# Performance work log

Measured on AMD Instinct MI355X. Metric: run time of the kernel, lower is better.

## Reference

```python
import jax, jax.numpy as jnp
import numpy as np
from jax import lax

N, CIN, H, W = 32, 128, 64, 64
COUT, KH, KW = 256, 3, 3
STRIDE = (1, 1)
PADDING = ((1, 1), (1, 1))


def setup_inputs() -> dict:
    key = jax.random.key(0)
    k1, k2, k3, k4 = jax.random.split(key, 4)
    # binary input in {0,1}
    x = jax.random.randint(k1, (N, CIN, H, W), 0, 2).astype(jnp.float32)
    # ternary weight in {-1,0,1}
    weight = (jax.random.randint(k2, (COUT, CIN, KH, KW), 0, 3) - 1).astype(jnp.float32)
    # integer bias (folded from BN, floored to int per get_sign_bias_from_bn)
    bias = jax.random.randint(k3, (COUT,), -200, 200).astype(jnp.float32)
    # sign in {-1,+1}, broadcast shape (1, COUT, 1, 1)
    sign = jnp.where(jax.random.bernoulli(k4, 0.5, (1, COUT, 1, 1)), 1.0, -1.0).astype(jnp.float32)
    return {"x": x, "weight": weight, "bias": bias, "sign": sign}


def reference(x, weight, bias, sign):
    # y = conv2d(x, W) + bias  (stride 1, pad 1, NCHW)
    y = lax.conv_general_dilated(
        x, weight,
        window_strides=STRIDE,
        padding=PADDING,
        dimension_numbers=("NCHW", "OIHW", "NCHW"),
    ) + bias[None, :, None, None]
    # rounding=True -> torch.round_(y)
    y = jnp.round(y)
    # output = 1 iff sign * y >= 0, cast back to input dtype
    return jnp.where(y * sign >= 0, jnp.float32(1), jnp.float32(0)).astype(x.dtype)
```

## Files before the change

### kernel.cpp

```cpp
#include <hip/hip_runtime.h>
#include <cstdint>


#define NIMG 32
#define CIN  128
#define HH   64
#define WW   64
#define COUT 256
#define PH   66
#define X4_ROW 4224
#define X4_IMG (PH * X4_ROW)
#define X4_BYTES ((size_t)NIMG * X4_IMG)
#define WQ4_BYTES ((size_t)9 * 8 * 2 * 64 * 16)

typedef int   v4i  __attribute__((ext_vector_type(4)));
typedef int   v8i  __attribute__((ext_vector_type(8)));
typedef float v16f __attribute__((ext_vector_type(16)));
typedef float v4f  __attribute__((ext_vector_type(4)));

__device__ __forceinline__ uint32_t pack4(uint32_t u) {
    const uint32_t tt = (u & 0x01010101u) << 1;
    return (tt & 0xFu) | ((tt >> 4) & 0xF0u) | ((tt >> 8) & 0xF00u)
         | ((tt >> 12) & 0xF000u);
}

__global__ __launch_bounds__(256) void xt_prepass(const float* __restrict__ x,
                                                  int8_t* __restrict__ xt4) {
    const int py = blockIdx.x;
    const int n  = blockIdx.y;
    const int t  = threadIdx.x;
    int8_t* rowbase = xt4 + (size_t)(n * PH + py) * X4_ROW;

    if (py == 0 || py == PH - 1) {
        int4 z = {0, 0, 0, 0};
        for (int j = t; j < X4_ROW / 16; j += 256)
            ((int4*)rowbase)[j] = z;
        return;
    }

    __shared__ __align__(16) int8_t Ls[64 * 144];
    const int y  = py - 1;
    const int xq = t & 15;
    const float4* xf = (const float4*)x;
#pragma unroll
    for (int j = 0; j < 8; ++j) {
        const int ci = (t >> 4) + j * 16;
        float4 v = xf[((size_t)(n * CIN + ci) * HH + y) * 16 + xq];
        const int xv = xq * 4;
        Ls[(xv + 0) * 144 + ci] = (int8_t)v.x;
        Ls[(xv + 1) * 144 + ci] = (int8_t)v.y;
        Ls[(xv + 2) * 144 + ci] = (int8_t)v.z;
        Ls[(xv + 3) * 144 + ci] = (int8_t)v.w;
    }
    __syncthreads();
    for (int j = t; j < 264; j += 256) {
        const int px = j >> 2;
        const int c  = j & 3;
        int4 o = {0, 0, 0, 0};
        if (px != 0 && px != PH - 1) {
            const int4* lp = (const int4*)&Ls[(px - 1) * 144 + c * 32];
            const int4 a = lp[0], b = lp[1];
            o.x = (int)(pack4((uint32_t)a.x) | (pack4((uint32_t)a.y) << 16));
            o.y = (int)(pack4((uint32_t)a.z) | (pack4((uint32_t)a.w) << 16));
            o.z = (int)(pack4((uint32_t)b.x) | (pack4((uint32_t)b.y) << 16));
            o.w = (int)(pack4((uint32_t)b.z) | (pack4((uint32_t)b.w) << 16));
        }
        *(int4*)(rowbase + (size_t)px * 64 + ((c ^ (px & 3)) << 4)) = o;
    }
}

__global__ __launch_bounds__(256) void w_prepack(const float* __restrict__ w,
                                                 int8_t* __restrict__ wq4) {
    const int idx = blockIdx.x * 256 + threadIdx.x;
    if (idx >= (int)WQ4_BYTES) return;
    const int b    = idx & 15;
    const int lane = (idx >> 4) & 63;
    const int s    = (idx >> 10) & 1;
    const int co32 = (idx >> 11) & 7;
    const int tap  = idx >> 14;
    const int co   = co32 * 32 + (lane & 31);
    const int ci0  = s * 64 + (lane >> 5) * 32 + b * 2;
    const int i0 = (int)w[(size_t)(co * CIN + ci0) * 9 + tap];
    const int i1 = (int)w[(size_t)(co * CIN + ci0 + 1) * 9 + tap];
    const uint32_t n0 = (i0 == 0) ? 0u : ((i0 > 0) ? 0x2u : 0xAu);
    const uint32_t n1 = (i1 == 0) ? 0u : ((i1 > 0) ? 0x2u : 0xAu);
    wq4[idx] = (int8_t)(n0 | (n1 << 4));
}

__device__ __forceinline__ void glds16(const void* g, uint32_t lds_off) {
    asm volatile("s_mov_b32 m0, %0\n"
                 "global_load_lds_dwordx4 %1, off"
                 :: "s"(lds_off), "v"(g) : "memory");
}

__device__ __forceinline__ v8i widen(v4i x) {
    v8i r = {x[0], x[1], x[2], x[3], 0, 0, 0, 0};
    return r;
}

__global__ __launch_bounds__(256) void binconv_gemm(
    const int8_t* __restrict__ xt4, const int8_t* __restrict__ wq4,
    const float* __restrict__ bias, const float* __restrict__ sign,
    float* __restrict__ out) {

    __shared__ __align__(16) int8_t Xraw[17 * 1024];

    const int t    = threadIdx.x;
    const int wid  = t >> 6;
    const int lane = t & 63;
    const int bx   = blockIdx.x;
    const int co0  = blockIdx.y * 128;
    const int n    = bx >> 5;
    const int y0   = (bx & 31) << 1;

    const int8_t* xbase = xt4 + (size_t)n * X4_IMG + (size_t)y0 * X4_ROW;
    {
        const int8_t* gsrc = xbase + lane * 16;
        const uint32_t lds0 = (uint32_t)(uintptr_t)Xraw;
        for (int j = wid; j < 17; j += 4)
            glds16(gsrc + j * 1024,
                   __builtin_amdgcn_readfirstlane(lds0 + j * 1024));
        asm volatile("s_waitcnt vmcnt(0)" ::: "memory");
        __syncthreads();
    }

    const int m_lo = lane & 31;
    const int hi   = lane >> 5;
    const int co_off = (wid >> 1) * 64;
    const int yw     = wid & 1;
    const int ct0    = (co0 + co_off) >> 5;

    const int8_t* Xw   = Xraw + yw * X4_ROW;
    const int8_t* wqb  = wq4 + lane * 16;

    v16f acc[2][2] = {};

#pragma unroll
    for (int tap = 0; tap < 9; ++tap) {
        const int ky = tap / 3, kx = tap % 3;
        const int8_t* xl = Xw + ky * X4_ROW;
        const int px0 = m_lo + kx;
        const int pk  = px0 & 3;

        v4i af[2][2];
#pragma unroll
        for (int c = 0; c < 2; ++c)
#pragma unroll
            for (int s = 0; s < 2; ++s)
                af[c][s] = *(const v4i*)(wqb
                    + ((((tap * 8 + ct0 + c) * 2) + s) << 10));

        v4i bf[2][2];
#pragma unroll
        for (int s = 0; s < 2; ++s) {
            const int sw = (((s << 1) + hi) ^ pk) << 4;
#pragma unroll
            for (int m = 0; m < 2; ++m)
                bf[m][s] = *(const v4i*)(xl + (px0 + m * 32) * 64 + sw);
        }
#pragma unroll
        for (int s = 0; s < 2; ++s)
#pragma unroll
            for (int c = 0; c < 2; ++c)
#pragma unroll
                for (int m = 0; m < 2; ++m)
                    acc[c][m] = __builtin_amdgcn_mfma_scale_f32_32x32x64_f8f6f4(
                        widen(af[c][s]), widen(bf[m][s]), acc[c][m],
                        4, 4,
                        0, 0x7F7F7F7F,
                        0, 0x7F7F7F7F);
    }

    __syncthreads();
    int8_t* Lep = Xraw + wid * 4096;

    const float* bco = bias + co0 + co_off;
    const float* sco = sign + co0 + co_off;
#pragma unroll
    for (int c = 0; c < 2; ++c) {
#pragma unroll
        for (int r = 0; r < 16; ++r) {
            const int co_l = c * 32 + (r & 3) + 8 * (r >> 2) + 4 * hi;
            const float bv = bco[co_l];
            const float sv = sco[co_l];
#pragma unroll
            for (int m = 0; m < 2; ++m) {
                const float yv = acc[c][m][r] + bv;
                const bool on = (sv > 0.0f) ? (yv >= 0.0f) : (yv <= 0.0f);
                Lep[co_l * 64 + m * 32 + m_lo] = (int8_t)on;
            }
        }
    }
    const int r16 = lane & 15, q4 = lane >> 4;
    float* outb = out + ((size_t)n * COUT + co0 + co_off) * (HH * WW)
                + (y0 + yw) * WW;
#pragma unroll
    for (int g = 0; g < 16; ++g) {
        const int p = g * 4 + q4;
        const uint32_t u = *(const uint32_t*)&Lep[p * 64 + r16 * 4];
        v4f v;
        v.x = (float)( u        & 0xff);
        v.y = (float)((u >>  8) & 0xff);
        v.z = (float)((u >> 16) & 0xff);
        v.w = (float)((u >> 24) & 0xff);
        __builtin_nontemporal_store(v,
            (v4f*)(outb + (size_t)p * (HH * WW) + r16 * 4));
    }
}

__global__ __launch_bounds__(256) void naive_conv(
    const float* __restrict__ x, const float* __restrict__ w,
    const float* __restrict__ bias, const float* __restrict__ sign,
    float* __restrict__ out) {
    const int idx = blockIdx.x * 256 + threadIdx.x;
    const int xc = idx & 63, y = (idx >> 6) & 63, co = (idx >> 12) & 255,
              n = idx >> 20;
    float s = 0.f;
    for (int ci = 0; ci < CIN; ++ci)
        for (int ky = 0; ky < 3; ++ky) {
            const int iy = y + ky - 1;
            if (iy < 0 || iy >= HH) continue;
            for (int kx = 0; kx < 3; ++kx) {
                const int ix = xc + kx - 1;
                if (ix < 0 || ix >= WW) continue;
                s += x[((size_t)(n * CIN + ci) * HH + iy) * WW + ix] *
                     w[((size_t)(co * CIN + ci) * 3 + ky) * 3 + kx];
            }
        }
    const float yv = s + bias[co];
    out[idx] = ((sign[co] > 0.f) ? (yv >= 0.f) : (yv <= 0.f)) ? 1.0f : 0.0f;
}

extern "C" void kernel_launch(void* const* d_in, const int* in_sizes, int n_in,
                              void* d_out, int out_size, void* d_ws, size_t ws_size,
                              hipStream_t stream) {
    const float* x    = (const float*)d_in[0];
    const float* w    = (const float*)d_in[1];
    const float* bias = (const float*)d_in[2];
    const float* sign = (const float*)d_in[3];
    float* out = (float*)d_out;

    const size_t need = X4_BYTES + WQ4_BYTES + 1024;
    if (ws_size < need) {
        naive_conv<<<dim3((NIMG * COUT * HH * WW) / 256), 256, 0, stream>>>(
            x, w, bias, sign, out);
        return;
    }
    int8_t* xt4 = (int8_t*)d_ws;
    int8_t* wq4 = (int8_t*)d_ws + X4_BYTES;

    xt_prepass<<<dim3(PH, NIMG), 256, 0, stream>>>(x, xt4);
    w_prepack<<<dim3((int)((WQ4_BYTES + 255) / 256)), 256, 0, stream>>>(w, wq4);
    binconv_gemm<<<dim3(NIMG * (HH / 2), COUT / 128), 256, 0, stream>>>(
        xt4, wq4, bias, sign, out);
}
```

Baseline: 209.3 us.

## Fuse input bit-packing prepass into conv GEMM kernel covering all output channels

Removes the separate xt_prepass kernel and its global fp4 staging buffer. Each 512-thread block now reads its four padded float input rows directly, converts them to fp4 codes in shared memory, and transposes them into the swizzled channel-packed layout. One block now computes all 256 output channels instead of two blocks of 128, so the shared input tile is reused across more output channels. The cost is that x rows are re-read by neighbouring blocks (halo overlap), and the in-LDS transpose does many scalar byte reads.

New measurement: 207.5 us. No clear change (-0.8%).

```diff
diff --git a/kernel.cpp b/kernel.cpp
--- a/kernel.cpp
+++ b/kernel.cpp
@@ -8,66 +8,16 @@
 #define WW   64
 #define COUT 256
 #define PH   66
-#define X4_ROW 4224
-#define X4_IMG (PH * X4_ROW)
-#define X4_BYTES ((size_t)NIMG * X4_IMG)
+#define X4ROW   4224
+#define STG_ROW 8704
+#define STG_BYTES (4 * STG_ROW)
+#define LDS_TOTAL (STG_BYTES + 4 * X4ROW)
 #define WQ4_BYTES ((size_t)9 * 8 * 2 * 64 * 16)
 
 typedef int   v4i  __attribute__((ext_vector_type(4)));
 typedef int   v8i  __attribute__((ext_vector_type(8)));
 typedef float v16f __attribute__((ext_vector_type(16)));
 typedef float v4f  __attribute__((ext_vector_type(4)));
-
-__device__ __forceinline__ uint32_t pack4(uint32_t u) {
-    const uint32_t tt = (u & 0x01010101u) << 1;
-    return (tt & 0xFu) | ((tt >> 4) & 0xF0u) | ((tt >> 8) & 0xF00u)
-         | ((tt >> 12) & 0xF000u);
-}
-
-__global__ __launch_bounds__(256) void xt_prepass(const float* __restrict__ x,
-                                                  int8_t* __restrict__ xt4) {
-    const int py = blockIdx.x;
-    const int n  = blockIdx.y;
-    const int t  = threadIdx.x;
-    int8_t* rowbase = xt4 + (size_t)(n * PH + py) * X4_ROW;
-
-    if (py == 0 || py == PH - 1) {
-        int4 z = {0, 0, 0, 0};
-        for (int j = t; j < X4_ROW / 16; j += 256)
-            ((int4*)rowbase)[j] = z;
-        return;
-    }
-
-    __shared__ __align__(16) int8_t Ls[64 * 144];
-    const int y  = py - 1;
-    const int xq = t & 15;
-    const float4* xf = (const float4*)x;
-#pragma unroll
-    for (int j = 0; j < 8; ++j) {
-        const int ci = (t >> 4) + j * 16;
-        float4 v = xf[((size_t)(n * CIN + ci) * HH + y) * 16 + xq];
-        const int xv = xq * 4;
-        Ls[(xv + 0) * 144 + ci] = (int8_t)v.x;
-        Ls[(xv + 1) * 144 + ci] = (int8_t)v.y;
-        Ls[(xv + 2) * 144 + ci] = (int8_t)v.z;
-        Ls[(xv + 3) * 144 + ci] = (int8_t)v.w;
-    }
-    __syncthreads();
-    for (int j = t; j < 264; j += 256) {
-        const int px = j >> 2;
-        const int c  = j & 3;
-        int4 o = {0, 0, 0, 0};
-        if (px != 0 && px != PH - 1) {
-            const int4* lp = (const int4*)&Ls[(px - 1) * 144 + c * 32];
-            const int4 a = lp[0], b = lp[1];
-            o.x = (int)(pack4((uint32_t)a.x) | (pack4((uint32_t)a.y) << 16));
-            o.y = (int)(pack4((uint32_t)a.z) | (pack4((uint32_t)a.w) << 16));
-            o.z = (int)(pack4((uint32_t)b.x) | (pack4((uint32_t)b.y) << 16));
-            o.w = (int)(pack4((uint32_t)b.z) | (pack4((uint32_t)b.w) << 16));
-        }
-        *(int4*)(rowbase + (size_t)px * 64 + ((c ^ (px & 3)) << 4)) = o;
-    }
-}
 
 __global__ __launch_bounds__(256) void w_prepack(const float* __restrict__ w,
                                                  int8_t* __restrict__ wq4) {
@@ -87,58 +37,100 @@
     wq4[idx] = (int8_t)(n0 | (n1 << 4));
 }
 
-__device__ __forceinline__ void glds16(const void* g, uint32_t lds_off) {
-    asm volatile("s_mov_b32 m0, %0\n"
-                 "global_load_lds_dwordx4 %1, off"
-                 :: "s"(lds_off), "v"(g) : "memory");
-}
-
 __device__ __forceinline__ v8i widen(v4i x) {
     v8i r = {x[0], x[1], x[2], x[3], 0, 0, 0, 0};
     return r;
 }
 
-__global__ __launch_bounds__(256) void binconv_gemm(
-    const int8_t* __restrict__ xt4, const int8_t* __restrict__ wq4,
+__global__ __launch_bounds__(512) void binconv_fused(
+    const float* __restrict__ x, const int8_t* __restrict__ wq4,
     const float* __restrict__ bias, const float* __restrict__ sign,
     float* __restrict__ out) {
 
-    __shared__ __align__(16) int8_t Xraw[17 * 1024];
-
-    const int t    = threadIdx.x;
+    __shared__ __align__(16) int8_t Smem[LDS_TOTAL];
+    int8_t* Stg = Smem;
+    int8_t* X4  = Smem + STG_BYTES;
+
+    const int t  = threadIdx.x;
+    const int bx = blockIdx.x;
+    const int n  = bx >> 5;
+    const int y0 = (bx & 31) << 1;
+
+    {
+        const int sy = t >> 7;
+        const int ci = t & 127;
+        const int y  = y0 + sy - 1;
+        uint32_t* sp = (uint32_t*)(Stg + sy * STG_ROW + ci * 68);
+        if (y >= 0 && y < HH) {
+            const float4* xr =
+                (const float4*)(x + (((size_t)n * CIN + ci) * HH + y) * WW);
+#pragma unroll
+            for (int q = 0; q < 16; ++q) {
+                float4 v = xr[q];
+                const uint32_t b0 = (__float_as_uint(v.x) >> 28) & 2u;
+                const uint32_t b1 = (__float_as_uint(v.y) >> 28) & 2u;
+                const uint32_t b2 = (__float_as_uint(v.z) >> 28) & 2u;
+                const uint32_t b3 = (__float_as_uint(v.w) >> 28) & 2u;
+                sp[q] = b0 | (b1 << 8) | (b2 << 16) | (b3 << 24);
+            }
+        } else {
+#pragma unroll
+            for (int q = 0; q < 16; ++q) sp[q] = 0u;
+        }
+    }
+    __syncthreads();
+
+    if (t < 264) {
+        const int sy  = t / 66;
+        const int pxp = t - sy * 66;
+        int8_t* dst = X4 + sy * X4ROW + pxp * 64;
+        if (pxp == 0 || pxp == 65) {
+            const int4 z = {0, 0, 0, 0};
+#pragma unroll
+            for (int c = 0; c < 4; ++c) *(int4*)(dst + c * 16) = z;
+        } else {
+            const int8_t* src = Stg + sy * STG_ROW + (pxp - 1);
+            uint32_t wrd[16];
+#pragma unroll
+            for (int k = 0; k < 16; ++k) {
+                uint32_t a = 0;
+#pragma unroll
+                for (int b = 0; b < 4; ++b) {
+                    const int j = k * 4 + b;
+                    const uint32_t lo = (uint8_t)src[(2 * j)     * 68];
+                    const uint32_t hi = (uint8_t)src[(2 * j + 1) * 68];
+                    a |= (lo | (hi << 4)) << (8 * b);
+                }
+                wrd[k] = a;
+            }
+            const int sk = pxp & 3;
+#pragma unroll
+            for (int c = 0; c < 4; ++c) {
+                int4 vv = {(int)wrd[c*4], (int)wrd[c*4+1],
+                           (int)wrd[c*4+2], (int)wrd[c*4+3]};
+                *(int4*)(dst + ((c ^ sk) << 4)) = vv;
+            }
+        }
+    }
+    __syncthreads();
+
     const int wid  = t >> 6;
     const int lane = t & 63;
-    const int bx   = blockIdx.x;
-    const int co0  = blockIdx.y * 128;
-    const int n    = bx >> 5;
-    const int y0   = (bx & 31) << 1;
-
-    const int8_t* xbase = xt4 + (size_t)n * X4_IMG + (size_t)y0 * X4_ROW;
-    {
-        const int8_t* gsrc = xbase + lane * 16;
-        const uint32_t lds0 = (uint32_t)(uintptr_t)Xraw;
-        for (int j = wid; j < 17; j += 4)
-            glds16(gsrc + j * 1024,
-                   __builtin_amdgcn_readfirstlane(lds0 + j * 1024));
-        asm volatile("s_waitcnt vmcnt(0)" ::: "memory");
-        __syncthreads();
-    }
-
     const int m_lo = lane & 31;
     const int hi   = lane >> 5;
     const int co_off = (wid >> 1) * 64;
     const int yw     = wid & 1;
-    const int ct0    = (co0 + co_off) >> 5;
-
-    const int8_t* Xw   = Xraw + yw * X4_ROW;
-    const int8_t* wqb  = wq4 + lane * 16;
+    const int ct0    = co_off >> 5;
+
+    const int8_t* Xw  = X4 + yw * X4ROW;
+    const int8_t* wqb = wq4 + lane * 16;
 
     v16f acc[2][2] = {};
 
 #pragma unroll
     for (int tap = 0; tap < 9; ++tap) {
         const int ky = tap / 3, kx = tap % 3;
-        const int8_t* xl = Xw + ky * X4_ROW;
+        const int8_t* xl = Xw + ky * X4ROW;
         const int px0 = m_lo + kx;
         const int pk  = px0 & 3;
 
@@ -171,11 +163,10 @@
                         0, 0x7F7F7F7F);
     }
 
-    __syncthreads();
-    int8_t* Lep = Xraw + wid * 4096;
-
-    const float* bco = bias + co0 + co_off;
-    const float* sco = sign + co0 + co_off;
+    int8_t* Lep = Smem + wid * 4096;
+
+    const float* bco = bias + co_off;
+    const float* sco = sign + co_off;
 #pragma unroll
     for (int c = 0; c < 2; ++c) {
 #pragma unroll
@@ -192,7 +183,7 @@
         }
     }
     const int r16 = lane & 15, q4 = lane >> 4;
-    float* outb = out + ((size_t)n * COUT + co0 + co_off) * (HH * WW)
+    float* outb = out + ((size_t)n * COUT + co_off) * (HH * WW)
                 + (y0 + yw) * WW;
 #pragma unroll
     for (int g = 0; g < 16; ++g) {
@@ -240,17 +231,14 @@
     const float* sign = (const float*)d_in[3];
     float* out = (float*)d_out;
 
-    const size_t need = X4_BYTES + WQ4_BYTES + 1024;
-    if (ws_size < need) {
+    if (ws_size < WQ4_BYTES) {
         naive_conv<<<dim3((NIMG * COUT * HH * WW) / 256), 256, 0, stream>>>(
             x, w, bias, sign, out);
         return;
     }
-    int8_t* xt4 = (int8_t*)d_ws;
-    int8_t* wq4 = (int8_t*)d_ws + X4_BYTES;
-
-    xt_prepass<<<dim3(PH, NIMG), 256, 0, stream>>>(x, xt4);
+    int8_t* wq4 = (int8_t*)d_ws;
+
     w_prepack<<<dim3((int)((WQ4_BYTES + 255) / 256)), 256, 0, stream>>>(w, wq4);
-    binconv_gemm<<<dim3(NIMG * (HH / 2), COUT / 128), 256, 0, stream>>>(
-        xt4, wq4, bias, sign, out);
-}
+    binconv_fused<<<dim3(NIMG * (HH / 2)), 512, 0, stream>>>(
+        x, wq4, bias, sign, out);
+}
```
